# Kernel optimization log

Hardware: AMD Instinct MI355X
Metric: run time of the kernel (lower is better)

The kernel has to match this reference:

```python
import jax, jax.numpy as jnp
import numpy as np

T, D, N, K, H = 4096, 2560, 8, 4, 256
QUERY_PRE_ATTN_SCALAR = 256.0
ROPE_THETA = 10000.0
RMS_EPS = 1e-6
SLIDING_WINDOW = 1024
NEG_INF = -1e30


def setup_inputs() -> dict:
    key = jax.random.key(0)
    ks = jax.random.split(key, 6)
    return {
        "x": jax.random.normal(ks[0], (T, D), dtype=jnp.float32),
        "wq": jax.random.normal(ks[1], (D, N, H), dtype=jnp.float32) * 0.02,
        "wk": jax.random.normal(ks[2], (D, K, H), dtype=jnp.float32) * 0.02,
        "wv": jax.random.normal(ks[3], (D, K, H), dtype=jnp.float32) * 0.02,
        "wo": jax.random.normal(ks[4], (N, H, D), dtype=jnp.float32) * 0.02,
        "q_norm_w": jnp.ones((H,), dtype=jnp.float32),
        "k_norm_w": jnp.ones((H,), dtype=jnp.float32),
        "positions": jnp.arange(T, dtype=jnp.int32),
    }


def rms_norm(x, w, eps=RMS_EPS):
    rms = jnp.sqrt(jnp.mean(x * x, axis=-1, keepdims=True) + eps)
    return w * (x / rms)


def apply_rope(x, positions, head_dim, theta):
    # x: [T, heads, H]; rotate-half RoPE
    half = head_dim // 2
    inv_freq = theta ** (-(jnp.arange(half, dtype=jnp.float32) * 2.0 / head_dim))
    ang = positions.astype(jnp.float32)[:, None] * inv_freq  # [T, half]
    sin = jnp.sin(ang)[:, None, :]
    cos = jnp.cos(ang)[:, None, :]
    x1, x2 = jnp.split(x, 2, axis=-1)
    return jnp.concatenate([x1 * cos - x2 * sin, x2 * cos + x1 * sin], axis=-1)


def reference(x, wq, wk, wv, wo, q_norm_w, k_norm_w, positions):
    # QKV projections (per-head)
    q = jnp.einsum('td,dnh->tnh', x, wq)            # [T, N, H]
    q = rms_norm(q, q_norm_w)
    q = q * (QUERY_PRE_ATTN_SCALAR ** -0.5)
    q = apply_rope(q, positions, H, ROPE_THETA)

    k = jnp.einsum('td,dkh->tkh', x, wk)            # [T, K, H]
    k = rms_norm(k, k_norm_w)
    k = apply_rope(k, positions, H, ROPE_THETA)

    v = jnp.einsum('td,dkh->tkh', x, wv)            # [T, K, H]

    # GQA sliding-window causal attention
    G = N // K
    qh = q.reshape(T, K, G, H)
    scores = jnp.einsum('tkgh,skh->kgts', qh, k)    # [K, G, T, T]
    pq = positions[:, None]
    pk = positions[None, :]
    mask = (pk <= pq) & (pq - pk < SLIDING_WINDOW)  # [T, T]
    scores = jnp.where(mask, scores, NEG_INF)
    p = jax.nn.softmax(scores, axis=-1)
    attn = jnp.einsum('kgts,skh->tkgh', p, v).reshape(T, N, H)

    o = jnp.einsum('tnh,nhd->td', attn, wo)         # [T, D]
    new_kv_cache = jnp.stack([k, v])                # [2, T, K, H]
    return new_kv_cache, o
```

## Files before the change

### kernel.cpp

```cpp
#include <hip/hip_runtime.h>
#include <stdint.h>

#define T_TOK 4096
#define DM    2560
#define NQ    8
#define NKV   4
#define HD    256
#define WIN   1024

using bf16x8 = __attribute__((ext_vector_type(8))) short;
using f32x4  = __attribute__((ext_vector_type(4))) float;
typedef unsigned short u16;

__device__ __forceinline__ u16 f2bf(float x) {
  union { float f; uint32_t u; } v; v.f = x;
  uint32_t u = v.u;
  return (u16)((u + 0x7fffu + ((u >> 16) & 1u)) >> 16);
}
__device__ __forceinline__ float bf2f(u16 b) {
  union { uint32_t u; float f; } v; v.u = ((uint32_t)b) << 16;
  return v.f;
}

__device__ __forceinline__ void async_cp16(const void* g, void* lds) {
  __builtin_amdgcn_global_load_lds(
      (const __attribute__((address_space(1))) uint32_t*)(uintptr_t)g,
      (__attribute__((address_space(3))) uint32_t*)(uint32_t)(uintptr_t)lds,
      16, 0, 0);
}

__global__ __launch_bounds__(256) void convert_f32_bf16(
    const float* __restrict__ in, u16* __restrict__ out, int n)
{
  for (int i = (blockIdx.x * 256 + threadIdx.x) * 4; i < n; i += gridDim.x * 256 * 4) {
    float4 v = *(const float4*)(in + i);
    ushort4 o;
    o.x = f2bf(v.x); o.y = f2bf(v.y); o.z = f2bf(v.z); o.w = f2bf(v.w);
    *(ushort4*)(out + i) = o;
  }
}

__global__ __launch_bounds__(256) void transpose_f32_bf16(
    const float* __restrict__ in, u16* __restrict__ out, int R, int C)
{
  __shared__ u16 tile[64][65];
  const int r0 = blockIdx.y * 64, c0 = blockIdx.x * 64;
  const int tr = threadIdx.x >> 6, tc = threadIdx.x & 63;
  #pragma unroll
  for (int i = 0; i < 16; ++i) {
    int r = tr + i * 4;
    tile[r][tc] = f2bf(in[(size_t)(r0 + r) * C + c0 + tc]);
  }
  __syncthreads();
  #pragma unroll
  for (int i = 0; i < 16; ++i) {
    int c = tr + i * 4;
    out[(size_t)(c0 + c) * R + r0 + tc] = tile[tc][c];
  }
}

template<int BM, int BN, bool F32OUT>
__global__ __launch_bounds__(512, 2) void gemm_t(
    const u16* __restrict__ A, const u16* __restrict__ B, void* __restrict__ Cv,
    int Kd, int lda, int ldb, int ldc, int MT)
{
  constexpr int MF = BM / 32;
  constexpr int NF = BN / 64;
  constexpr int ISS = (BM + BN) / 64;
  constexpr int AISS = BM / 64;
  __shared__ __align__(16) u16 lds[2][(BM + BN) * 64];
  const int tid = threadIdx.x;
  const int wave = tid >> 6, lane = tid & 63;
  const int lg = lane >> 4, lc = lane & 15;
  const int wr = wave >> 2, wc = wave & 3;
  const int nwg = gridDim.x, bid = blockIdx.x;
  const int nid = (bid & 7) * (nwg >> 3) + (bid >> 3);
  const int m0 = (nid % MT) * BM, n0 = (nid / MT) * BN;
  const int NT = Kd >> 6;

  const int srow = tid >> 3;
  const int scol = ((tid & 7) * 16) ^ ((srow & 7) << 4);
  const u16* Ag = A + (size_t)(m0 + srow) * lda + (scol >> 1);
  const u16* Bg = B + (size_t)(n0 + srow) * ldb + (scol >> 1);
  char* lds0 = (char*)&lds[0][0];
  char* lds1 = (char*)&lds[1][0];

  #define STAGE_T(LD, KT) do {                                              \
    const int kc_ = (KT) * 64;                                              \
    _Pragma("unroll")                                                       \
    for (int li = 0; li < ISS; ++li) {                                      \
      if (li < AISS)                                                        \
        async_cp16(Ag + (size_t)(li * 64) * lda + kc_,                      \
                   (LD) + li * 8192 + wave * 1024);                         \
      else                                                                  \
        async_cp16(Bg + (size_t)((li - AISS) * 64) * ldb + kc_,             \
                   (LD) + li * 8192 + wave * 1024);                         \
    }                                                                       \
  } while (0)

  #define WAIT_ISS() do {                                                   \
    if (ISS == 8) asm volatile("s_waitcnt vmcnt(8)" ::: "memory");          \
    else          asm volatile("s_waitcnt vmcnt(7)" ::: "memory");          \
  } while (0)

  const f32x4 zf = {0.f, 0.f, 0.f, 0.f};
  f32x4 acc[MF][NF];
  #pragma unroll
  for (int i = 0; i < MF; ++i)
    #pragma unroll
    for (int j = 0; j < NF; ++j) acc[i][j] = zf;

  STAGE_T(lds0, 0);
  STAGE_T(lds1, 1);
  WAIT_ISS();
  __builtin_amdgcn_s_barrier();
  __builtin_amdgcn_sched_barrier(0);

  for (int t = 0; t < NT; ++t) {
    const int cur = t & 1;
    const char* Ab = cur ? lds1 : lds0;
    const char* Bb = Ab + BM * 128;

    bf16x8 bf[NF][2];
    #pragma unroll
    for (int j = 0; j < NF; ++j)
      #pragma unroll
      for (int k2 = 0; k2 < 2; ++k2) {
        const int row = wc * (BN / 4) + j * 16 + lc;
        const int cb = k2 * 64 + lg * 16;
        bf[j][k2] = *(const bf16x8*)(Bb + row * 128 + (cb ^ ((row & 7) << 4)));
      }

    #pragma unroll
    for (int p = 0; p < MF / 2; ++p) {
      bf16x8 af[2][2];
      #pragma unroll
      for (int im = 0; im < 2; ++im)
        #pragma unroll
        for (int k2 = 0; k2 < 2; ++k2) {
          const int row = wr * (BM / 2) + (p * 2 + im) * 16 + lc;
          const int cb = k2 * 64 + lg * 16;
          af[im][k2] = *(const bf16x8*)(Ab + row * 128 + (cb ^ ((row & 7) << 4)));
        }
      __builtin_amdgcn_s_setprio(1);
      #pragma unroll
      for (int im = 0; im < 2; ++im)
        #pragma unroll
        for (int j = 0; j < NF; ++j)
          #pragma unroll
          for (int k2 = 0; k2 < 2; ++k2)
            acc[p * 2 + im][j] = __builtin_amdgcn_mfma_f32_16x16x32_bf16(
                af[im][k2], bf[j][k2], acc[p * 2 + im][j], 0, 0, 0);
      __builtin_amdgcn_s_setprio(0);
    }

    __builtin_amdgcn_s_barrier();
    __builtin_amdgcn_sched_barrier(0);
    int nk = t + 2; if (nk > NT - 1) nk = NT - 1;
    if (cur == 0) { STAGE_T(lds0, nk); } else { STAGE_T(lds1, nk); }
    WAIT_ISS();
    __builtin_amdgcn_s_barrier();
    __builtin_amdgcn_sched_barrier(0);
  }
  #undef STAGE_T
  #undef WAIT_ISS

  #pragma unroll
  for (int i = 0; i < MF; ++i)
    #pragma unroll
    for (int j = 0; j < NF; ++j)
      #pragma unroll
      for (int r = 0; r < 4; ++r) {
        const int row = m0 + wr * (BM / 2) + i * 16 + lg * 4 + r;
        const int col = n0 + wc * (BN / 4) + j * 16 + lc;
        if (F32OUT) ((float*)Cv)[(size_t)row * ldc + col] = acc[i][j][r];
        else        ((u16*)Cv)[(size_t)row * ldc + col] = f2bf(acc[i][j][r]);
      }
}

__global__ __launch_bounds__(256) void fuse_norm_rope(
    const u16* __restrict__ qkv, const float* __restrict__ qnw, const float* __restrict__ knw,
    const int* __restrict__ pos, u16* __restrict__ qb, u16* __restrict__ kb,
    u16* __restrict__ vb, float* __restrict__ kvout)
{
  const int t = blockIdx.x;
  const int wave = threadIdx.x >> 6, lane = threadIdx.x & 63;
  const float p = (float)pos[t];
  const float kf = 0.10381025296523007f;
  float s0, c0, s1, c1;
  sincosf(p * exp2f(-(float)lane * kf), &s0, &c0);
  sincosf(p * exp2f(-(float)(lane + 64) * kf), &s1, &c1);
  const u16* row = qkv + (size_t)t * 4096;

  for (int pp = 0; pp < 4; ++pp) {
    const int hr = pp * 4 + wave;
    if (hr >= 12) {
      const int kk = hr - 12;
      const u16* src = row + 3072 + kk * 256;
      float* dstf = kvout + (size_t)T_TOK * NKV * HD + ((size_t)t * NKV + kk) * HD;
      u16*   dstb = vb + ((size_t)t * NKV + kk) * HD;
      #pragma unroll
      for (int q4 = 0; q4 < 4; ++q4) {
        const u16 s = src[lane + q4 * 64];
        dstf[lane + q4 * 64] = bf2f(s);
        dstb[lane + q4 * 64] = s;
      }
    } else {
      const bool isq = hr < 8;
      const int cb = isq ? hr * 256 : 2048 + (hr - 8) * 256;
      float v0 = bf2f(row[cb + lane]);
      float v1 = bf2f(row[cb + lane + 64]);
      float v2 = bf2f(row[cb + lane + 128]);
      float v3 = bf2f(row[cb + lane + 192]);
      float ss = v0 * v0 + v1 * v1 + v2 * v2 + v3 * v3;
      #pragma unroll
      for (int off = 1; off < 64; off <<= 1) ss += __shfl_xor(ss, off);
      float sc = rsqrtf(ss * (1.0f / 256.0f) + 1e-6f);
      if (isq) sc *= 0.0625f;
      const float* wn = isq ? qnw : knw;
      v0 *= sc * wn[lane];
      v1 *= sc * wn[lane + 64];
      v2 *= sc * wn[lane + 128];
      v3 *= sc * wn[lane + 192];
      const float n0 = v0 * c0 - v2 * s0;
      const float n2 = v2 * c0 + v0 * s0;
      const float n1 = v1 * c1 - v3 * s1;
      const float n3 = v3 * c1 + v1 * s1;
      if (isq) {
        u16* dst = qb + (size_t)t * 2048 + hr * 256;
        dst[lane]       = f2bf(n0);
        dst[lane + 64]  = f2bf(n1);
        dst[lane + 128] = f2bf(n2);
        dst[lane + 192] = f2bf(n3);
      } else {
        const int kk = hr - 8;
        float* dstf = kvout + ((size_t)t * NKV + kk) * HD;
        dstf[lane]       = n0;
        dstf[lane + 64]  = n1;
        dstf[lane + 128] = n2;
        dstf[lane + 192] = n3;
        u16* dstb = kb + ((size_t)t * NKV + kk) * HD;
        dstb[lane]       = f2bf(n0);
        dstb[lane + 64]  = f2bf(n1);
        dstb[lane + 128] = f2bf(n2);
        dstb[lane + 192] = f2bf(n3);
      }
    }
  }
}

__global__ __launch_bounds__(256) void transpose_v(
    const u16* __restrict__ vc, u16* __restrict__ vt)
{
  __shared__ u16 tile[64][65];
  const int kk = blockIdx.z;
  const int t0 = blockIdx.y * 64, h0 = blockIdx.x * 64;
  const int tr = threadIdx.x >> 6, tc = threadIdx.x & 63;
  #pragma unroll
  for (int i = 0; i < 16; ++i) {
    int tt = tr + i * 4;
    tile[tt][tc] = vc[((size_t)(t0 + tt) * NKV + kk) * HD + h0 + tc];
  }
  __syncthreads();
  #pragma unroll
  for (int i = 0; i < 16; ++i) {
    int h = tr + i * 4;
    vt[(size_t)kk * HD * T_TOK + (size_t)(h0 + h) * T_TOK + t0 + tc] = tile[tc][h];
  }
}

__global__ __launch_bounds__(512, 1) void attn_kernel(
    const u16* __restrict__ qb, const u16* __restrict__ kc,
    const u16* __restrict__ vt, u16* __restrict__ ob)
{
  __shared__ __align__(16) u16 Ks[2][64 * 256];
  __shared__ __align__(16) u16 Vts[2][256 * 64];
  __shared__ __align__(16) u16 Ps[8][16 * 64];

  const int kk = blockIdx.y;
  const int t0 = blockIdx.x * 64;
  const int tid = threadIdx.x;
  const int wave = tid >> 6, lane = tid & 63;
  const int lg = lane >> 4, lc = lane & 15;
  const int hq = kk * 2 + (wave >> 2);
  const int wrow = (wave & 3) * 16;
  const int lswz = (lc & 7) << 4;
  const f32x4 zf = {0.f, 0.f, 0.f, 0.f};

  const int lrowK = tid >> 5;
  const int scolK = ((tid & 31) * 16) ^ ((lrowK & 7) << 4);
  const int lrowV = tid >> 3;
  const int scolV = ((tid & 7) * 16) ^ ((lrowV & 7) << 4);

  #define STAGEKV(KT, BUF) do {                                                \
    const int kb_ = (KT) * 64;                                                 \
    const u16* kp_ = kc + (size_t)(kb_ + lrowK) * (NKV * HD) + kk * HD + (scolK >> 1); \
    _Pragma("unroll")                                                          \
    for (int is = 0; is < 4; ++is)                                             \
      async_cp16(kp_ + (size_t)(is * 16) * (NKV * HD),                         \
                 (char*)&Ks[BUF][0] + is * 8192 + wave * 1024);                \
    const u16* vp_ = vt + (size_t)kk * (HD * T_TOK) + (size_t)lrowV * T_TOK + kb_ + (scolV >> 1); \
    _Pragma("unroll")                                                          \
    for (int is = 0; is < 4; ++is)                                             \
      async_cp16(vp_ + (size_t)(is * 64) * T_TOK,                              \
                 (char*)&Vts[BUF][0] + is * 8192 + wave * 1024);               \
  } while (0)

  bf16x8 qf[8];
  {
    const u16* qp = qb + (size_t)(t0 + wrow + lc) * 2048 + hq * 256 + lg * 8;
    #pragma unroll
    for (int ks = 0; ks < 8; ++ks) qf[ks] = *(const bf16x8*)(qp + ks * 32);
  }

  f32x4 o_acc[16];
  #pragma unroll
  for (int j = 0; j < 16; ++j) o_acc[j] = zf;
  float m_r[4], l_r[4];
  #pragma unroll
  for (int r = 0; r < 4; ++r) { m_r[r] = -1e30f; l_r[r] = 0.f; }

  const int mtile = t0 >> 6;
  const int ktf = (mtile >= 16) ? (mtile - 16) : 0;

  STAGEKV(ktf, 0);
  __syncthreads();

  int cur = 0;
  for (int kt = ktf; kt <= mtile; ++kt) {
    const int kb = kt * 64;
    if (kt < mtile) STAGEKV(kt + 1, cur ^ 1);

    const u16* Kb = &Ks[cur][0];
    const u16* Vb = &Vts[cur][0];

    f32x4 sf[4];
    #pragma unroll
    for (int j = 0; j < 4; ++j) sf[j] = zf;
    __builtin_amdgcn_s_setprio(1);
    #pragma unroll
    for (int ks = 0; ks < 8; ++ks)
      #pragma unroll
      for (int j = 0; j < 4; ++j) {
        const int row = j * 16 + lc;
        bf16x8 kf = *(const bf16x8*)((const char*)Kb + ((row * 512 + ks * 64 + lg * 16) ^ lswz));
        sf[j] = __builtin_amdgcn_mfma_f32_16x16x32_bf16(qf[ks], kf, sf[j], 0, 0, 0);
      }
    __builtin_amdgcn_s_setprio(0);

    const bool interior = (kb >= t0 - 960) && (kb <= t0 - 64);
    if (!interior) {
      #pragma unroll
      for (int j = 0; j < 4; ++j) {
        const int gcol = kb + j * 16 + lc;
        #pragma unroll
        for (int r = 0; r < 4; ++r) {
          const int grow = t0 + wrow + lg * 4 + r;
          if ((unsigned)(grow - gcol) >= WIN) sf[j][r] = -1e30f;
        }
      }
    }

    float a_r[4];
    #pragma unroll
    for (int r = 0; r < 4; ++r) {
      float v = fmaxf(fmaxf(sf[0][r], sf[1][r]), fmaxf(sf[2][r], sf[3][r]));
      v = fmaxf(v, __shfl_xor(v, 1));
      v = fmaxf(v, __shfl_xor(v, 2));
      v = fmaxf(v, __shfl_xor(v, 4));
      v = fmaxf(v, __shfl_xor(v, 8));
      const float mn = fmaxf(m_r[r], v);
      a_r[r] = __expf(m_r[r] - mn);
      m_r[r] = mn;
    }

    char* myP = (char*)&Ps[wave][0];
    #pragma unroll
    for (int r = 0; r < 4; ++r) {
      const int row = lg * 4 + r;
      const int rsw = (row & 7) << 4;
      float su = 0.f;
      #pragma unroll
      for (int j = 0; j < 4; ++j) {
        const float p = __expf(sf[j][r] - m_r[r]);
        su += p;
        *(u16*)(myP + ((row * 128 + (j * 16 + lc) * 2) ^ rsw)) = f2bf(p);
      }
      su += __shfl_xor(su, 1);
      su += __shfl_xor(su, 2);
      su += __shfl_xor(su, 4);
      su += __shfl_xor(su, 8);
      l_r[r] = l_r[r] * a_r[r] + su;
    }

    #pragma unroll
    for (int j = 0; j < 16; ++j) {
      o_acc[j][0] *= a_r[0];
      o_acc[j][1] *= a_r[1];
      o_acc[j][2] *= a_r[2];
      o_acc[j][3] *= a_r[3];
    }

    bf16x8 pa[2];
    #pragma unroll
    for (int ks = 0; ks < 2; ++ks)
      pa[ks] = *(const bf16x8*)(myP + ((lc * 128 + ks * 64 + lg * 16) ^ lswz));
    __builtin_amdgcn_s_setprio(1);
    #pragma unroll
    for (int ks = 0; ks < 2; ++ks)
      #pragma unroll
      for (int j = 0; j < 16; ++j) {
        const int row = j * 16 + lc;
        bf16x8 vf = *(const bf16x8*)((const char*)Vb + ((row * 128 + ks * 64 + lg * 16) ^ lswz));
        o_acc[j] = __builtin_amdgcn_mfma_f32_16x16x32_bf16(pa[ks], vf, o_acc[j], 0, 0, 0);
      }
    __builtin_amdgcn_s_setprio(0);

    __syncthreads();
    cur ^= 1;
  }
  #undef STAGEKV

  #pragma unroll
  for (int r = 0; r < 4; ++r) {
    const float li = 1.f / l_r[r];
    const size_t rowb = (size_t)(t0 + wrow + lg * 4 + r) * 2048 + hq * 256 + lc;
    #pragma unroll
    for (int j = 0; j < 16; ++j)
      ob[rowb + j * 16] = f2bf(o_acc[j][r] * li);
  }
}

extern "C" void kernel_launch(void* const* d_in, const int* in_sizes, int n_in,
                              void* d_out, int out_size, void* d_ws, size_t ws_size,
                              hipStream_t stream)
{
  (void)in_sizes; (void)n_in; (void)out_size; (void)ws_size;
  const float* x   = (const float*)d_in[0];
  const float* wq  = (const float*)d_in[1];
  const float* wk  = (const float*)d_in[2];
  const float* wv  = (const float*)d_in[3];
  const float* wo  = (const float*)d_in[4];
  const float* qnw = (const float*)d_in[5];
  const float* knw = (const float*)d_in[6];
  const int*   pos = (const int*)d_in[7];
  float* out = (float*)d_out;

  char* ws = (char*)d_ws;
  u16* woT   = (u16*)(ws);
  u16* xb    = (u16*)(ws + 10485760);
  u16* wqkvT = (u16*)(ws + 31457280);
  u16* qkv   = (u16*)(ws + 52428800);
  u16* q_b   = xb;
  u16* kb    = wqkvT;
  u16* vb    = (u16*)(ws + 31457280 + 8388608);
  u16* vtb   = qkv;
  u16* attn  = (u16*)(ws + 52428800 + 8388608);

  convert_f32_bf16<<<2048, 256, 0, stream>>>(x, xb, T_TOK * DM);
  transpose_f32_bf16<<<dim3(32, 40), 256, 0, stream>>>(wq, wqkvT, DM, 2048);
  transpose_f32_bf16<<<dim3(16, 40), 256, 0, stream>>>(wk, wqkvT + 2048 * DM, DM, 1024);
  transpose_f32_bf16<<<dim3(16, 40), 256, 0, stream>>>(wv, wqkvT + 3072 * DM, DM, 1024);
  transpose_f32_bf16<<<dim3(40, 32), 256, 0, stream>>>(wo, woT, 2048, DM);

  gemm_t<256, 256, false><<<256, 512, 0, stream>>>(xb, wqkvT, qkv, DM, DM, DM, 4096, 16);

  fuse_norm_rope<<<T_TOK, 256, 0, stream>>>(qkv, qnw, knw, pos, q_b, kb, vb, out);

  transpose_v<<<dim3(4, 64, 4), 256, 0, stream>>>(vb, vtb);

  attn_kernel<<<dim3(64, 4), 512, 0, stream>>>(q_b, kb, vtb, attn);

  gemm_t<128, 320, true><<<256, 512, 0, stream>>>(attn, woT, out + 2 * (size_t)T_TOK * NKV * HD,
                                                  2048, 2048, 2048, DM, 32);
}
```

Before: 262.9 us.

## Add 256x256 QKV GEMM with interleaved LDS staging and MFMA

Adds a dedicated 256x256 bf16 GEMM for the QKV projection. It uses double-buffered LDS with a prefetch distance of two K-tiles and splits each tile's staging into B and two A halves, interleaved with four MFMA quarter-phases and raised wave priority during MFMA. The goal is to hide global-to-LDS latency behind matrix work within one workgroup per CU. The tradeoff is 128KB of LDS and launch_bounds(512,1), so only one workgroup fits per CU. The many barriers could also add stalls.

```diff
diff --git a/kernel.cpp b/kernel.cpp
--- a/kernel.cpp
+++ b/kernel.cpp
@@ -57,6 +57,134 @@
     int c = tr + i * 4;
     out[(size_t)(c0 + c) * R + r0 + tc] = tile[tc][c];
   }
+}
+
+template<bool F32OUT>
+__global__ __launch_bounds__(512, 1) void gemm256p(
+    const u16* __restrict__ A, const u16* __restrict__ B, void* __restrict__ Cv,
+    int Kd, int lda, int ldb, int ldc)
+{
+  __shared__ __align__(16) u16 lds[2][2][256 * 64];
+  const int tid = threadIdx.x;
+  const int wave = tid >> 6, lane = tid & 63;
+  const int lg = lane >> 4, lc = lane & 15;
+  const int wr = wave >> 2, wc = wave & 3;
+  const int nwg = gridDim.x, bid = blockIdx.x;
+  const int nid = (bid & 7) * (nwg >> 3) + (bid >> 3);
+  const int m0 = (nid & 15) * 256, n0 = (nid >> 4) * 256;
+  const int NT = Kd >> 6;
+
+  const int srow = tid >> 3;
+  const int scol = ((tid & 7) * 16) ^ ((srow & 7) << 4);
+  const u16* Ag = A + (size_t)(m0 + srow) * lda + (scol >> 1);
+  const u16* Bg = B + (size_t)(n0 + srow) * ldb + (scol >> 1);
+
+  #define STAGE_B4(BUF, KT) do {                                              \
+    const int kc_ = (KT) * 64;                                                \
+    _Pragma("unroll")                                                         \
+    for (int li = 0; li < 4; ++li)                                            \
+      async_cp16(Bg + (size_t)(li * 64) * ldb + kc_,                          \
+                 (char*)&lds[BUF][1][0] + li * 8192 + wave * 1024);           \
+  } while (0)
+  #define STAGE_A2(BUF, KT, H) do {                                           \
+    const int kc_ = (KT) * 64;                                                \
+    async_cp16(Ag + (size_t)((H) * 64) * lda + kc_,                           \
+               (char*)&lds[BUF][0][0] + (H) * 8192 + wave * 1024);            \
+    async_cp16(Ag + (size_t)((H) * 64 + 128) * lda + kc_,                     \
+               (char*)&lds[BUF][0][0] + ((H) + 2) * 8192 + wave * 1024);      \
+  } while (0)
+
+  #define LOAD_AF(P) do {                                                     \
+    _Pragma("unroll")                                                         \
+    for (int im = 0; im < 2; ++im)                                            \
+      _Pragma("unroll")                                                       \
+      for (int k2 = 0; k2 < 2; ++k2) {                                        \
+        const int row = wr * 128 + ((P) * 2 + im) * 16 + lc;                  \
+        const int cb = k2 * 64 + lg * 16;                                     \
+        af[im][k2] = *(const bf16x8*)(Ab + row * 128 + (cb ^ ((row & 7) << 4))); \
+      }                                                                       \
+  } while (0)
+  #define MFMA_Q(P) do {                                                      \
+    __builtin_amdgcn_s_setprio(1);                                            \
+    _Pragma("unroll")                                                         \
+    for (int im = 0; im < 2; ++im)                                            \
+      _Pragma("unroll")                                                       \
+      for (int j = 0; j < 4; ++j)                                             \
+        _Pragma("unroll")                                                     \
+        for (int k2 = 0; k2 < 2; ++k2)                                        \
+          acc[(P) * 2 + im][j] = __builtin_amdgcn_mfma_f32_16x16x32_bf16(     \
+              af[im][k2], bfr[j][k2], acc[(P) * 2 + im][j], 0, 0, 0);         \
+    __builtin_amdgcn_s_setprio(0);                                            \
+  } while (0)
+  #define LGKM0_BAR() do {                                                    \
+    asm volatile("s_waitcnt lgkmcnt(0)" ::: "memory");                        \
+    __builtin_amdgcn_s_barrier();                                             \
+    __builtin_amdgcn_sched_barrier(0);                                        \
+  } while (0)
+
+  const f32x4 zf = {0.f, 0.f, 0.f, 0.f};
+  f32x4 acc[8][4];
+  #pragma unroll
+  for (int i = 0; i < 8; ++i)
+    #pragma unroll
+    for (int j = 0; j < 4; ++j) acc[i][j] = zf;
+
+  STAGE_B4(0, 0); STAGE_A2(0, 0, 0); STAGE_A2(0, 0, 1);
+  STAGE_B4(1, 1); STAGE_A2(1, 1, 0); STAGE_A2(1, 1, 1);
+  asm volatile("s_waitcnt vmcnt(8)" ::: "memory");
+  __builtin_amdgcn_s_barrier();
+  __builtin_amdgcn_sched_barrier(0);
+
+  for (int t = 0; t < NT; ++t) {
+    const int cur = t & 1;
+    const char* Ab = (const char*)&lds[cur][0][0];
+    const char* Bb = (const char*)&lds[cur][1][0];
+    int nk = t + 2; if (nk > NT - 1) nk = NT - 1;
+
+    bf16x8 bfr[4][2], af[2][2];
+    #pragma unroll
+    for (int j = 0; j < 4; ++j)
+      #pragma unroll
+      for (int k2 = 0; k2 < 2; ++k2) {
+        const int row = wc * 64 + j * 16 + lc;
+        const int cb = k2 * 64 + lg * 16;
+        bfr[j][k2] = *(const bf16x8*)(Bb + row * 128 + (cb ^ ((row & 7) << 4)));
+      }
+    LOAD_AF(0);
+    LGKM0_BAR();
+    STAGE_B4(cur, nk);
+    MFMA_Q(0);
+    LOAD_AF(1);
+    LGKM0_BAR();
+    STAGE_A2(cur, nk, 0);
+    MFMA_Q(1);
+    LOAD_AF(2);
+    MFMA_Q(2);
+    LOAD_AF(3);
+    LGKM0_BAR();
+    STAGE_A2(cur, nk, 1);
+    MFMA_Q(3);
+    asm volatile("s_waitcnt vmcnt(8)" ::: "memory");
+    __builtin_amdgcn_s_barrier();
+    __builtin_amdgcn_sched_barrier(0);
+  }
+  #undef STAGE_B4
+  #undef STAGE_A2
+  #undef LOAD_AF
+  #undef MFMA_Q
+  #undef LGKM0_BAR
+
+  #pragma unroll
+  for (int i = 0; i < 8; ++i)
+    #pragma unroll
+    for (int j = 0; j < 4; ++j)
+      #pragma unroll
+      for (int r = 0; r < 4; ++r) {
+        const int row = m0 + wr * 128 + i * 16 + lg * 4 + r;
+        const int col = n0 + wc * 64 + j * 16 + lc;
+        if (F32OUT) ((float*)Cv)[(size_t)row * ldc + col] = acc[i][j][r];
+        else        ((u16*)Cv)[(size_t)row * ldc + col] = f2bf(acc[i][j][r]);
+      }
 }
 
 template<int BM, int BN, bool F32OUT>
@@ -463,7 +591,7 @@
   transpose_f32_bf16<<<dim3(16, 40), 256, 0, stream>>>(wv, wqkvT + 3072 * DM, DM, 1024);
   transpose_f32_bf16<<<dim3(40, 32), 256, 0, stream>>>(wo, woT, 2048, DM);
 
-  gemm_t<256, 256, false><<<256, 512, 0, stream>>>(xb, wqkvT, qkv, DM, DM, DM, 4096, 16);
+  gemm256p<false><<<256, 512, 0, stream>>>(xb, wqkvT, qkv, DM, DM, DM, 4096);
 
   fuse_norm_rope<<<T_TOK, 256, 0, stream>>>(qkv, qnw, knw, pos, q_b, kb, vb, out);
 
```

New measurement: 251.5 us. -4.4%, faster.
